# Optimization experiments

Measured on AMD Instinct MI355X. Metric: run time of the kernel, lower is better.

## Reference

```python
import jax, jax.numpy as jnp
import numpy as np

N = 100_000      # nodes
E = 3_200_000    # edges (avg degree 32)
F_IN = 128       # num_features
DIM = 10         # hidden dim (module default)
B = 1000         # graphs in the batch


def setup_inputs() -> dict:
    key = jax.random.key(0)
    k1, k2, k3, k4, k5, k6 = jax.random.split(key, 6)
    x = jax.random.normal(k1, (N, F_IN), dtype=jnp.float32)
    edge_index = jax.random.randint(k2, (2, E), 0, N)
    batch = jnp.sort(jax.random.randint(k3, (N,), 0, B))
    # SAGEConv with concat=True has weight shape [2*in, out], no bias
    W1 = jax.random.normal(k4, (2 * F_IN, DIM), dtype=jnp.float32) * 0.05
    W2 = jax.random.normal(k5, (2 * DIM, DIM), dtype=jnp.float32) * 0.1
    Wfc = jax.random.normal(k6, (DIM, 1), dtype=jnp.float32) * 0.1
    return {"x": x, "edge_index": edge_index, "batch": batch,
            "W1": W1, "W2": W2, "Wfc": Wfc}


def _segment_mean(vals, idx, num_segments):
    s = jax.ops.segment_sum(vals, idx, num_segments=num_segments)
    c = jax.ops.segment_sum(jnp.ones((vals.shape[0],), vals.dtype), idx,
                            num_segments=num_segments)
    return s / jnp.maximum(c, 1.0)[:, None]


def _sage_conv(x, src, dst, W):
    # message = x[src]; mean-aggregate into dst; cat([x, aggr]) @ W
    aggr = _segment_mean(x[src], dst, N)          # [N, F]
    return jnp.concatenate([x, aggr], axis=-1) @ W  # [N, out]


def reference(x, edge_index, batch, W1, W2, Wfc):
    src, dst = edge_index[0], edge_index[1]
    h = jax.nn.relu(_sage_conv(x, src, dst, W1))   # [N, DIM]
    h = _sage_conv(h, src, dst, W2)                # [N, DIM]
    g = _segment_mean(h, batch, B)                 # [B, DIM] global_mean_pool
    return jax.nn.sigmoid(g @ Wfc)                 # [B, 1]
```

## Files before the change

kernel.cpp:

```cpp
#include <hip/hip_runtime.h>
#include <cstdint>

typedef unsigned int u32;
typedef unsigned short u16;

#define N_NODES 100000
#define N_EDGES 3200000
#define F_IN 128
#define DIM 10
#define QB 16
#define B_GRAPHS 1000
#define FRONT_T 512
#define NBLK_N 196

#define SHIFTC 7
#define NBINS 128
#define NCB 782
#define CAPC 4608
#define CHUNK_C 8192
#define NBLK_C 391
#define GSTRIDE 16
#define SEGW 129

__device__ __forceinline__ u16 f2b(float f) {
  union { float f; u32 i; } c; c.f = f;
  u32 r = c.i + 0x7FFFu + ((c.i >> 16) & 1u);
  return (u16)(r >> 16);
}
__device__ __forceinline__ float bl(u32 u) {
  union { u32 i; float f; } c; c.i = u << 16; return c.f;
}
__device__ __forceinline__ float bh(u32 u) {
  union { u32 i; float f; } c; c.i = u & 0xFFFF0000u; return c.f;
}

__device__ __forceinline__ void gemm_body(
    int bid, int tid,
    const float* __restrict__ x, const float* __restrict__ W,
    float* __restrict__ p1, u16* __restrict__ q1b)
{
  int i = bid * FRONT_T + tid;
  if (i >= N_NODES) return;
  const float4* __restrict__ xr = (const float4*)(x + (size_t)i * F_IN);
  float ap[DIM], aq[DIM];
  #pragma unroll
  for (int j = 0; j < DIM; ++j) { ap[j] = 0.f; aq[j] = 0.f; }
  #pragma unroll 4
  for (int k4 = 0; k4 < F_IN / 4; ++k4) {
    float4 v = xr[k4];
    const float* __restrict__ w0 = W + (k4 * 4) * DIM;
    const float* __restrict__ w1 = W + (F_IN + k4 * 4) * DIM;
    #pragma unroll
    for (int j = 0; j < DIM; ++j) {
      ap[j] += v.x * w0[j] + v.y * w0[DIM + j] + v.z * w0[2 * DIM + j] + v.w * w0[3 * DIM + j];
      aq[j] += v.x * w1[j] + v.y * w1[DIM + j] + v.z * w1[2 * DIM + j] + v.w * w1[3 * DIM + j];
    }
  }
  float* pr = p1 + (size_t)i * DIM;
  #pragma unroll
  for (int j = 0; j < DIM; ++j) pr[j] = ap[j];
  u32* qr = (u32*)(q1b + (size_t)i * QB);
  uint4 v0; u32 v1;
  v0.x = (u32)f2b(aq[0]) | ((u32)f2b(aq[1]) << 16);
  v0.y = (u32)f2b(aq[2]) | ((u32)f2b(aq[3]) << 16);
  v0.z = (u32)f2b(aq[4]) | ((u32)f2b(aq[5]) << 16);
  v0.w = (u32)f2b(aq[6]) | ((u32)f2b(aq[7]) << 16);
  v1   = (u32)f2b(aq[8]) | ((u32)f2b(aq[9]) << 16);
  *(uint4*)qr = v0;
  qr[4] = v1;
}

__device__ __forceinline__ void coarse_body(
    int bid, int tid,
    const int* __restrict__ src, const int* __restrict__ dst,
    u32* __restrict__ gcurc, u32* __restrict__ coarse)
{
  __shared__ u32 srt[CHUNK_C];
  __shared__ u32 segst[NCB + 1];
  __shared__ u32 rank[NCB];
  __shared__ u32 gbase[NCB];
  __shared__ u32 wtot[4];

  for (int t = tid; t < NCB; t += FRONT_T) rank[t] = 0u;
  __syncthreads();

  int base = bid * CHUNK_C;
  const int4* __restrict__ dst4 = (const int4*)dst;
  const int4* __restrict__ src4 = (const int4*)src;
  #pragma unroll
  for (int it = 0; it < CHUNK_C / (FRONT_T * 4); ++it) {
    int e = base + it * (FRONT_T * 4) + tid * 4;
    if (e < N_EDGES) {
      int4 d = dst4[(base >> 2) + it * FRONT_T + tid];
      atomicAdd(&rank[(u32)d.x >> SHIFTC], 1u);
      atomicAdd(&rank[(u32)d.y >> SHIFTC], 1u);
      atomicAdd(&rank[(u32)d.z >> SHIFTC], 1u);
      atomicAdd(&rank[(u32)d.w >> SHIFTC], 1u);
    }
  }
  __syncthreads();

  if (tid < 256) {
    u32 lh[4] = {0u, 0u, 0u, 0u};
    u32 lsum = 0u;
    if (tid < 196) {
      #pragma unroll
      for (int k = 0; k < 4; ++k) {
        int b4 = tid * 4 + k;
        lh[k] = (b4 < NCB) ? rank[b4] : 0u;
        lsum += lh[k];
      }
    }
    u32 v = lsum;
    #pragma unroll
    for (int off = 1; off < 64; off <<= 1) {
      u32 t = __shfl_up(v, off, 64);
      if ((tid & 63) >= off) v += t;
    }
    if ((tid & 63) == 63) wtot[tid >> 6] = v;
    __syncthreads();
    u32 wofs = 0u;
    #pragma unroll
    for (int w = 0; w < 3; ++w) if ((tid >> 6) > w) wofs += wtot[w];
    if (tid < 196) {
      u32 excl = wofs + v - lsum;
      #pragma unroll
      for (int k = 0; k < 4; ++k) {
        int b4 = tid * 4 + k;
        if (b4 < NCB) segst[b4] = excl;
        excl += lh[k];
      }
      if (tid == 195) segst[NCB] = excl;
    }
  } else {
    __syncthreads();
  }
  __syncthreads();

  for (int t = tid; t < NCB; t += FRONT_T) {
    u32 c = segst[t + 1] - segst[t];
    gbase[t] = c ? atomicAdd(&gcurc[t * GSTRIDE], c) : 0u;
    rank[t] = 0u;
  }
  __syncthreads();

  #pragma unroll
  for (int it = 0; it < CHUNK_C / (FRONT_T * 4); ++it) {
    int e = base + it * (FRONT_T * 4) + tid * 4;
    if (e < N_EDGES) {
      int4 d = dst4[(base >> 2) + it * FRONT_T + tid];
      int4 s = src4[(base >> 2) + it * FRONT_T + tid];
      #pragma unroll
      for (int q = 0; q < 4; ++q) {
        u32 dd = (u32)((q == 0) ? d.x : (q == 1) ? d.y : (q == 2) ? d.z : d.w);
        u32 ss = (u32)((q == 0) ? s.x : (q == 1) ? s.y : (q == 2) ? s.z : s.w);
        u32 cb = dd >> SHIFTC;
        u32 pos = segst[cb] + atomicAdd(&rank[cb], 1u);
        srt[pos] = ((dd & (NBINS - 1u)) << 17) | ss;
      }
    }
  }
  __syncthreads();

  int grp = tid >> 4, lane = tid & 15;
  for (int cb = grp; cb < NCB; cb += FRONT_T / 16) {
    u32 st = segst[cb];
    u32 cnt = segst[cb + 1] - st;
    u32 gb = gbase[cb];
    for (u32 r = lane; r < cnt; r += 16u) {
      u32 p = gb + r;
      if (p < CAPC)
        coarse[(size_t)cb * CAPC + p] = srt[st + r];
    }
  }
}

__global__ __launch_bounds__(FRONT_T) void k_front(
    const int* __restrict__ src, const int* __restrict__ dst,
    u32* __restrict__ gcurc, u32* __restrict__ coarse,
    const float* __restrict__ x, const float* __restrict__ W,
    float* __restrict__ p1, u16* __restrict__ q1b)
{
  if (blockIdx.x < NBLK_C)
    coarse_body(blockIdx.x, threadIdx.x, src, dst, gcurc, coarse);
  else
    gemm_body(blockIdx.x - NBLK_C, threadIdx.x, x, W, p1, q1b);
}

#define SEG_GATHER(QSRC)                                                      \
  float s[DIM];                                                               \
  _Pragma("unroll")                                                           \
  for (int j = 0; j < DIM; ++j) s[j] = 0.f;                                   \
  {                                                                           \
    int k = st + l;                                                           \
    for (; k + 8 < en; k += 16) {                                             \
      int s0 = (int)srt[k], s1 = (int)srt[k + 8];                             \
      const u32* __restrict__ q0 = (const u32*)(QSRC + (size_t)s0 * QB);      \
      const u32* __restrict__ q1 = (const u32*)(QSRC + (size_t)s1 * QB);      \
      uint4 A0 = *(const uint4*)q0; u32 B0 = q0[4];                           \
      uint4 A1 = *(const uint4*)q1; u32 B1 = q1[4];                           \
      s[0] += bl(A0.x) + bl(A1.x); s[1] += bh(A0.x) + bh(A1.x);               \
      s[2] += bl(A0.y) + bl(A1.y); s[3] += bh(A0.y) + bh(A1.y);               \
      s[4] += bl(A0.z) + bl(A1.z); s[5] += bh(A0.z) + bh(A1.z);               \
      s[6] += bl(A0.w) + bl(A1.w); s[7] += bh(A0.w) + bh(A1.w);               \
      s[8] += bl(B0) + bl(B1);     s[9] += bh(B0) + bh(B1);                   \
    }                                                                         \
    if (k < en) {                                                             \
      int s0 = (int)srt[k];                                                   \
      const u32* __restrict__ q0 = (const u32*)(QSRC + (size_t)s0 * QB);      \
      uint4 A0 = *(const uint4*)q0; u32 B0 = q0[4];                           \
      s[0] += bl(A0.x); s[1] += bh(A0.x);                                     \
      s[2] += bl(A0.y); s[3] += bh(A0.y);                                     \
      s[4] += bl(A0.z); s[5] += bh(A0.z);                                     \
      s[6] += bl(A0.w); s[7] += bh(A0.w);                                     \
      s[8] += bl(B0);   s[9] += bh(B0);                                       \
    }                                                                         \
  }                                                                           \
  _Pragma("unroll")                                                           \
  for (int m = 1; m < 8; m <<= 1) {                                           \
    _Pragma("unroll")                                                         \
    for (int j = 0; j < DIM; ++j) s[j] += __shfl_xor(s[j], m, 8);             \
  }

__global__ __launch_bounds__(512) void k_lay1(
    const u32* __restrict__ gcurc, u32* __restrict__ coarse,
    const float* __restrict__ p1, const u16* __restrict__ q1b,
    const float* __restrict__ W2, const float* __restrict__ Wfc,
    float* __restrict__ y, float* __restrict__ z,
    u32* __restrict__ segg)
{
  __shared__ u32 lrec[CAPC];
  __shared__ u32 srt[CAPC];
  __shared__ u32 hist[NBINS];
  __shared__ u32 segst[NBINS + 1];
  __shared__ u32 rank[NBINS];
  __shared__ u32 wtot[2];
  __shared__ float wv[2 * DIM];
  int tid = threadIdx.x;
  int c = blockIdx.x;
  if (tid < 2 * DIM) {
    float sacc = 0.f;
    #pragma unroll
    for (int j = 0; j < DIM; ++j) sacc += W2[tid * DIM + j] * Wfc[j];
    wv[tid] = sacc;
  }
  if (tid < NBINS) { hist[tid] = 0u; rank[tid] = 0u; }
  __syncthreads();
  int n = min((int)gcurc[c * GSTRIDE], CAPC);
  const u32* __restrict__ rc = coarse + (size_t)c * CAPC;
  for (int r = tid; r < n; r += 512) {
    u32 v = rc[r];
    lrec[r] = v;
    atomicAdd(&hist[(v >> 17) & (NBINS - 1u)], 1u);
  }
  __syncthreads();
  if (tid < NBINS) {
    u32 h = hist[tid];
    u32 v = h;
    #pragma unroll
    for (int off = 1; off < 64; off <<= 1) {
      u32 t = __shfl_up(v, off, 64);
      if ((tid & 63) >= off) v += t;
    }
    if ((tid & 63) == 63) wtot[tid >> 6] = v;
    segst[tid] = v - h;
  }
  __syncthreads();
  if (tid >= 64 && tid < NBINS) segst[tid] += wtot[0];
  if (tid == 0) segst[NBINS] = wtot[0] + wtot[1];
  __syncthreads();
  for (int r = tid; r < n; r += 512) {
    u32 v = lrec[r];
    u32 dl = (v >> 17) & (NBINS - 1u);
    u32 pos = segst[dl] + atomicAdd(&rank[dl], 1u);
    srt[pos] = v & 0x1FFFFu;
  }
  __syncthreads();
  for (int r = tid; r < n; r += 512) coarse[(size_t)c * CAPC + r] = srt[r];
  if (tid <= NBINS) segg[(size_t)c * SEGW + tid] = segst[tid];
  int g0 = tid >> 3, l = tid & 7;
  #pragma unroll
  for (int rd = 0; rd < 2; ++rd) {
    int g2 = rd * 64 + g0;
    int st = (int)segst[g2], en = (int)segst[g2 + 1];
    SEG_GATHER(q1b)
    if (l == 0) {
      int i = c * NBINS + g2;
      if (i < N_NODES) {
        float dinv = 1.0f / fmaxf((float)(en - st), 1.0f);
        const float* __restrict__ pr = p1 + (size_t)i * DIM;
        float yv = 0.f, zv = 0.f;
        #pragma unroll
        for (int j = 0; j < DIM; ++j) {
          float h = fmaxf(pr[j] + s[j] * dinv, 0.0f);
          yv += h * wv[j];
          zv += h * wv[DIM + j];
        }
        y[i] = yv;
        z[i] = zv;
      }
    }
  }
}

__global__ __launch_bounds__(256) void k_zpool(
    const u32* __restrict__ coarse, const u32* __restrict__ segg,
    const float* __restrict__ y, const float* __restrict__ z,
    const int* __restrict__ batch, float* __restrict__ out)
{
  __shared__ float wsum[4];
  int g = blockIdx.x;
  int tid = threadIdx.x;
  int lo = 0, hi = N_NODES;
  while (lo < hi) { int m = (lo + hi) >> 1; if (batch[m] < g) lo = m + 1; else hi = m; }
  int start = lo;
  hi = N_NODES;
  while (lo < hi) { int m = (lo + hi) >> 1; if (batch[m] < g + 1) lo = m + 1; else hi = m; }
  int end = lo;
  int grp = tid >> 3, l = tid & 7;
  float acc = 0.f;
  for (int i = start + grp; i < end; i += 32) {
    int c = i >> SHIFTC, bin = i & (NBINS - 1);
    u32 st = segg[(size_t)c * SEGW + bin];
    u32 en = segg[(size_t)c * SEGW + bin + 1];
    const u32* __restrict__ rc = coarse + (size_t)c * CAPC;
    float sc = 0.f;
    for (u32 k = st + l; k < en; k += 8u) sc += z[rc[k]];
    #pragma unroll
    for (int m = 1; m < 8; m <<= 1) sc += __shfl_xor(sc, m, 8);
    if (l == 0) acc += y[i] + sc / fmaxf((float)(en - st), 1.0f);
  }
  if (l != 0) acc = 0.f;
  #pragma unroll
  for (int m = 1; m < 64; m <<= 1) acc += __shfl_xor(acc, m, 64);
  if ((tid & 63) == 0) wsum[tid >> 6] = acc;
  __syncthreads();
  if (tid == 0) {
    float tot = wsum[0] + wsum[1] + wsum[2] + wsum[3];
    float gm = tot / fmaxf((float)(end - start), 1.0f);
    out[g] = 1.0f / (1.0f + expf(-gm));
  }
}

extern "C" void kernel_launch(void* const* d_in, const int* in_sizes, int n_in,
                              void* d_out, int out_size, void* d_ws, size_t ws_size,
                              hipStream_t stream)
{
  const float* x     = (const float*)d_in[0];
  const int*   ei    = (const int*)d_in[1];
  const int*   batch = (const int*)d_in[2];
  const float* W1    = (const float*)d_in[3];
  const float* W2    = (const float*)d_in[4];
  const float* Wfc   = (const float*)d_in[5];
  float* out = (float*)d_out;

  const int* src = ei;
  const int* dst = ei + N_EDGES;

  u32* wsp = (u32*)d_ws;
  u32* gcurc  = wsp;
  u32* coarse = wsp + 12544;
  u32* segg   = coarse + (size_t)NCB * CAPC;
  u32* after  = segg + 100928;
  u16*   q1b = (u16*)after;
  float* p1  = (float*)(after + 800000);
  float* y   = (float*)(after + 1800000);
  float* z   = (float*)(after + 1900096);

  hipMemsetAsync(gcurc, 0, (size_t)NCB * GSTRIDE * sizeof(u32), stream);

  k_front<<<NBLK_C + NBLK_N, FRONT_T, 0, stream>>>(src, dst, gcurc, coarse,
                                                   x, W1, p1, q1b);
  k_lay1<<<NCB, 512, 0, stream>>>(gcurc, coarse, p1, q1b, W2, Wfc, y, z, segg);
  k_zpool<<<B_GRAPHS, 256, 0, stream>>>(coarse, segg, y, z, batch, out);
}
```

Measured before the change: 195.1 us.

## Replace global atomic bucket scatter with per-chunk sorted runs gathered by consumers

The front pass no longer reserves space in each coarse bucket with global atomics and scatters records into them. Each chunk block now writes its locally sorted records contiguously, along with a per-chunk segment table. The layer kernel runs a prefix scan over the 391 chunk counts to find the offsets of its bucket's slices, then gathers them into shared memory. This removes the memset and the contended global atomics, and makes the front-pass writes coalesced. In exchange, the consumer does scattered reads of 391 small slices per bucket, plus a 512-wide scan with many barriers.

```diff
diff --git a/kernel.cpp b/kernel.cpp
--- a/kernel.cpp
+++ b/kernel.cpp
@@ -19,8 +19,8 @@
 #define CAPC 4608
 #define CHUNK_C 8192
 #define NBLK_C 391
-#define GSTRIDE 16
 #define SEGW 129
+#define TW (NCB + 1)
 
 __device__ __forceinline__ u16 f2b(float f) {
   union { float f; u32 i; } c; c.f = f;
@@ -73,12 +73,11 @@
 __device__ __forceinline__ void coarse_body(
     int bid, int tid,
     const int* __restrict__ src, const int* __restrict__ dst,
-    u32* __restrict__ gcurc, u32* __restrict__ coarse)
+    u32* __restrict__ rec, u32* __restrict__ segt)
 {
   __shared__ u32 srt[CHUNK_C];
   __shared__ u32 segst[NCB + 1];
   __shared__ u32 rank[NCB];
-  __shared__ u32 gbase[NCB];
   __shared__ u32 wtot[4];
 
   for (int t = tid; t < NCB; t += FRONT_T) rank[t] = 0u;
@@ -137,11 +136,7 @@
   }
   __syncthreads();
 
-  for (int t = tid; t < NCB; t += FRONT_T) {
-    u32 c = segst[t + 1] - segst[t];
-    gbase[t] = c ? atomicAdd(&gcurc[t * GSTRIDE], c) : 0u;
-    rank[t] = 0u;
-  }
+  for (int t = tid; t < NCB; t += FRONT_T) rank[t] = 0u;
   __syncthreads();
 
   #pragma unroll
@@ -162,27 +157,21 @@
   }
   __syncthreads();
 
-  int grp = tid >> 4, lane = tid & 15;
-  for (int cb = grp; cb < NCB; cb += FRONT_T / 16) {
-    u32 st = segst[cb];
-    u32 cnt = segst[cb + 1] - st;
-    u32 gb = gbase[cb];
-    for (u32 r = lane; r < cnt; r += 16u) {
-      u32 p = gb + r;
-      if (p < CAPC)
-        coarse[(size_t)cb * CAPC + p] = srt[st + r];
-    }
-  }
+  for (int k = tid; k <= NCB; k += FRONT_T)
+    segt[(size_t)bid * TW + k] = segst[k];
+  int total = (int)segst[NCB];
+  for (int t = tid; t < total; t += FRONT_T)
+    rec[base + t] = srt[t];
 }
 
 __global__ __launch_bounds__(FRONT_T) void k_front(
     const int* __restrict__ src, const int* __restrict__ dst,
-    u32* __restrict__ gcurc, u32* __restrict__ coarse,
+    u32* __restrict__ rec, u32* __restrict__ segt,
     const float* __restrict__ x, const float* __restrict__ W,
     float* __restrict__ p1, u16* __restrict__ q1b)
 {
   if (blockIdx.x < NBLK_C)
-    coarse_body(blockIdx.x, threadIdx.x, src, dst, gcurc, coarse);
+    coarse_body(blockIdx.x, threadIdx.x, src, dst, rec, segt);
   else
     gemm_body(blockIdx.x - NBLK_C, threadIdx.x, x, W, p1, q1b);
 }
@@ -223,11 +212,11 @@
   }
 
 __global__ __launch_bounds__(512) void k_lay1(
-    const u32* __restrict__ gcurc, u32* __restrict__ coarse,
+    const u32* __restrict__ rec, const u32* __restrict__ segt,
     const float* __restrict__ p1, const u16* __restrict__ q1b,
     const float* __restrict__ W2, const float* __restrict__ Wfc,
     float* __restrict__ y, float* __restrict__ z,
-    u32* __restrict__ segg)
+    u32* __restrict__ sortrec, u32* __restrict__ segg)
 {
   __shared__ u32 lrec[CAPC];
   __shared__ u32 srt[CAPC];
@@ -235,6 +224,8 @@
   __shared__ u32 segst[NBINS + 1];
   __shared__ u32 rank[NBINS];
   __shared__ u32 wtot[2];
+  __shared__ u32 bst[NBLK_C];
+  __shared__ u32 ntot_s;
   __shared__ float wv[2 * DIM];
   int tid = threadIdx.x;
   int c = blockIdx.x;
@@ -245,13 +236,37 @@
     wv[tid] = sacc;
   }
   if (tid < NBINS) { hist[tid] = 0u; rank[tid] = 0u; }
-  __syncthreads();
-  int n = min((int)gcurc[c * GSTRIDE], CAPC);
-  const u32* __restrict__ rc = coarse + (size_t)c * CAPC;
-  for (int r = tid; r < n; r += 512) {
-    u32 v = rc[r];
-    lrec[r] = v;
-    atomicAdd(&hist[(v >> 17) & (NBINS - 1u)], 1u);
+  u32 cnt = 0u;
+  if (tid < NBLK_C)
+    cnt = segt[(size_t)tid * TW + c + 1] - segt[(size_t)tid * TW + c];
+  srt[tid] = cnt;
+  __syncthreads();
+  for (int off = 1; off < 512; off <<= 1) {
+    u32 v = (tid >= off) ? srt[tid - off] : 0u;
+    __syncthreads();
+    if (tid >= off) srt[tid] += v;
+    __syncthreads();
+  }
+  if (tid < NBLK_C) bst[tid] = srt[tid] - cnt;
+  if (tid == NBLK_C - 1) ntot_s = srt[tid];
+  __syncthreads();
+  int n = min((int)ntot_s, CAPC);
+  {
+    int grp = tid >> 3, l = tid & 7;
+    for (int b = grp; b < NBLK_C; b += 64) {
+      u32 s0 = segt[(size_t)b * TW + c];
+      u32 cn = segt[(size_t)b * TW + c + 1] - s0;
+      const u32* __restrict__ rp = rec + (size_t)b * CHUNK_C + s0;
+      u32 bb = bst[b];
+      for (u32 r = l; r < cn; r += 8u) {
+        u32 pos = bb + r;
+        if (pos < (u32)CAPC) {
+          u32 v = rp[r];
+          lrec[pos] = v;
+          atomicAdd(&hist[(v >> 17) & (NBINS - 1u)], 1u);
+        }
+      }
+    }
   }
   __syncthreads();
   if (tid < NBINS) {
@@ -276,7 +291,7 @@
     srt[pos] = v & 0x1FFFFu;
   }
   __syncthreads();
-  for (int r = tid; r < n; r += 512) coarse[(size_t)c * CAPC + r] = srt[r];
+  for (int r = tid; r < n; r += 512) sortrec[(size_t)c * CAPC + r] = srt[r];
   if (tid <= NBINS) segg[(size_t)c * SEGW + tid] = segst[tid];
   int g0 = tid >> 3, l = tid & 7;
   #pragma unroll
@@ -304,7 +319,7 @@
 }
 
 __global__ __launch_bounds__(256) void k_zpool(
-    const u32* __restrict__ coarse, const u32* __restrict__ segg,
+    const u32* __restrict__ sortrec, const u32* __restrict__ segg,
     const float* __restrict__ y, const float* __restrict__ z,
     const int* __restrict__ batch, float* __restrict__ out)
 {
@@ -323,7 +338,7 @@
     int c = i >> SHIFTC, bin = i & (NBINS - 1);
     u32 st = segg[(size_t)c * SEGW + bin];
     u32 en = segg[(size_t)c * SEGW + bin + 1];
-    const u32* __restrict__ rc = coarse + (size_t)c * CAPC;
+    const u32* __restrict__ rc = sortrec + (size_t)c * CAPC;
     float sc = 0.f;
     for (u32 k = st + l; k < en; k += 8u) sc += z[rc[k]];
     #pragma unroll
@@ -358,19 +373,19 @@
   const int* dst = ei + N_EDGES;
 
   u32* wsp = (u32*)d_ws;
-  u32* gcurc  = wsp;
-  u32* coarse = wsp + 12544;
-  u32* segg   = coarse + (size_t)NCB * CAPC;
-  u32* after  = segg + 100928;
+  u32* rec     = wsp;
+  u32* segt    = rec + (size_t)NBLK_C * CHUNK_C;
+  u32* sortrec = segt + 306176;
+  u32* segg    = sortrec + (size_t)NCB * CAPC;
+  u32* after   = segg + 100928;
   u16*   q1b = (u16*)after;
   float* p1  = (float*)(after + 800000);
   float* y   = (float*)(after + 1800000);
   float* z   = (float*)(after + 1900096);
 
-  hipMemsetAsync(gcurc, 0, (size_t)NCB * GSTRIDE * sizeof(u32), stream);
-
-  k_front<<<NBLK_C + NBLK_N, FRONT_T, 0, stream>>>(src, dst, gcurc, coarse,
+  k_front<<<NBLK_C + NBLK_N, FRONT_T, 0, stream>>>(src, dst, rec, segt,
                                                    x, W1, p1, q1b);
-  k_lay1<<<NCB, 512, 0, stream>>>(gcurc, coarse, p1, q1b, W2, Wfc, y, z, segg);
-  k_zpool<<<B_GRAPHS, 256, 0, stream>>>(coarse, segg, y, z, batch, out);
-}
+  k_lay1<<<NCB, 512, 0, stream>>>(rec, segt, p1, q1b, W2, Wfc, y, z,
+                                  sortrec, segg);
+  k_zpool<<<B_GRAPHS, 256, 0, stream>>>(sortrec, segg, y, z, batch, out);
+}
```

Result: faster. 185.6 us (median of 2 runs) (-4.8%).
